# Optimization experiments

Hardware: AMD Instinct MI355X
Metric: run time of the kernel (lower is better)

Reference implementation:

```python
import jax, jax.numpy as jnp
import numpy as np

TEMPERATURE = 8.0  # sqrt(d_k=64)

def setup_inputs() -> dict:
    key = jax.random.key(0)
    kq, kk, kv = jax.random.split(key, 3)
    B, S, D = 32, 2048, 64  # B = batch*heads
    q = jax.random.normal(kq, (B, S, D), dtype=jnp.float32)
    k = jax.random.normal(kk, (B, S, D), dtype=jnp.float32)
    v = jax.random.normal(kv, (B, S, D), dtype=jnp.float32)
    return {"q": q, "k": k, "v": v}

def reference(q, k, v):
    # attn = softmax((q @ k^T) / temperature) along key dim; dropout = identity (eval)
    attn = jnp.einsum('bqd,bkd->bqk', q, k) / TEMPERATURE  # [B, S, S]
    attn = jax.nn.softmax(attn, axis=2)
    out = jnp.einsum('bqk,bkd->bqd', attn, v)              # [B, S, D]
    return out
```

## Files before the change

kernel.cpp:

```cpp
#include <hip/hip_runtime.h>
#include <stdint.h>


#define BATCH 32
#define SEQ   2048
#define DIM   64
#define QBLK_WAVE 32
#define NWAVES 4
#define QBLK  (QBLK_WAVE*NWAVES)
#define KVBLK 64
#define NT    (SEQ/KVBLK)
#define BUFSHORTS (KVBLK*DIM)

typedef __attribute__((ext_vector_type(8)))  __bf16   bf16x8;
typedef __attribute__((ext_vector_type(2)))  __bf16   bf16x2;
typedef __attribute__((ext_vector_type(16))) float    f32x16;
typedef __attribute__((ext_vector_type(2)))  unsigned uint2v;
typedef __attribute__((ext_vector_type(4)))  unsigned uint4v;

static __device__ __forceinline__ unsigned pk(float lo, float hi) {
    bf16x2 p; p[0] = (__bf16)lo; p[1] = (__bf16)hi;
    return __builtin_bit_cast(unsigned, p);
}
static __device__ __forceinline__ float exp2v(float x) {
    float r; asm("v_exp_f32 %0, %1" : "=v"(r) : "v"(x)); return r;
}
static __device__ __forceinline__ float max3(float a, float b, float c) {
    float d; asm("v_max3_f32 %0, %1, %2, %3" : "=v"(d) : "v"(a), "v"(b), "v"(c));
    return d;
}
static __device__ __forceinline__ float other_half(float v, int hi) {
    unsigned u = __builtin_bit_cast(unsigned, v);
    uint2v r = __builtin_amdgcn_permlane32_swap(u, u, false, false);
    return __builtin_bit_cast(float, hi ? r[0] : r[1]);
}

#define MFMA32(A, B, C) __builtin_amdgcn_mfma_f32_32x32x16_bf16((A), (B), (C), 0, 0, 0)
#define TRR(dst, OFFSTR) \
    asm volatile("ds_read_b64_tr_b16 %0, %1 offset:" OFFSTR : "=v"(dst) : "v"(trb))
#define SUM4(a,b,c,d) (((a)+(b)) + ((c)+(d)))

static __device__ __forceinline__ bf16x8 frag_of(uint2v r0, uint2v r1) {
    uint4v w = { r0[0], r0[1], r1[0], r1[1] };
    return __builtin_bit_cast(bf16x8, w);
}

__global__ __launch_bounds__(256, 2)
void attn_fwd_kernel(const float* __restrict__ q,
                     const float* __restrict__ k,
                     const float* __restrict__ v,
                     float* __restrict__ out)
{
    __shared__ unsigned short Ksh[2][BUFSHORTS];
    __shared__ unsigned short Vsh[2][BUFSHORTS];

    const int id    = blockIdx.x;
    const int swz   = (id & 7) * ((SEQ / QBLK) * BATCH / 8) + (id >> 3);
    const int batch = swz >> 4;
    const int qtile = swz & 15;

    const int t    = threadIdx.x;
    const int lane = t & 63;
    const int wid  = t >> 6;
    const int hi   = lane >> 5;
    const int l31  = lane & 31;
    const int l7   = lane & 7;

    const size_t bbase = (size_t)batch * SEQ * DIM;
    const int q0w = qtile * QBLK + wid * QBLK_WAVE;

    bf16x8 qf[4];
    {
        const float sc = 0.125f * 1.44269504088896341f;
        const float* qp = q + bbase + (size_t)(q0w + l31) * DIM + hi * 8;
        #pragma unroll
        for (int dblk = 0; dblk < 4; ++dblk) {
            float4 f0 = *(const float4*)(qp + dblk * 16);
            float4 f1 = *(const float4*)(qp + dblk * 16 + 4);
            uint4v w = { pk(f0.x * sc, f0.y * sc), pk(f0.z * sc, f0.w * sc),
                         pk(f1.x * sc, f1.y * sc), pk(f1.z * sc, f1.w * sc) };
            qf[dblk] = __builtin_bit_cast(bf16x8, w);
        }
    }
    asm("" : "+v"(qf[0]), "+v"(qf[1]), "+v"(qf[2]), "+v"(qf[3]));

    const int srow = t >> 2, sq = t & 3;
    const float* kg = k + bbase + (size_t)srow * DIM + sq * 16;
    const float* vg = v + bbase + (size_t)srow * DIM + sq * 16;
    const int ch0 = ((2 * sq)     ^ (srow & 7)) * 8;
    const int ch1 = ((2 * sq + 1) ^ (srow & 7)) * 8;

    const int bq = (l31 & 15) >> 2, ee = (lane >> 4) & 1, cc = lane & 3;
    const unsigned vb = (unsigned)(uintptr_t)&Vsh[0][0];
    const unsigned trbase = vb + (unsigned)((8 * hi + bq) * 128 +
                                            (((2 * ee + (cc >> 1)) ^ bq) * 16) + (cc & 1) * 8);

    f32x16 oacc0, oacc1;
    #pragma unroll
    for (int r = 0; r < 16; ++r) { oacc0[r] = 0.f; oacc1[r] = 0.f; }
    float m_run = 0.0f, l_run = 0.0f;

    float4 rk[4], rv[4];
    #pragma unroll
    for (int i = 0; i < 4; ++i) {
        rk[i] = *(const float4*)(kg + i * 4);
        rv[i] = *(const float4*)(vg + i * 4);
    }
    {
        uint4v kw0 = { pk(rk[0].x, rk[0].y), pk(rk[0].z, rk[0].w),
                       pk(rk[1].x, rk[1].y), pk(rk[1].z, rk[1].w) };
        uint4v kw1 = { pk(rk[2].x, rk[2].y), pk(rk[2].z, rk[2].w),
                       pk(rk[3].x, rk[3].y), pk(rk[3].z, rk[3].w) };
        uint4v vw0 = { pk(rv[0].x, rv[0].y), pk(rv[0].z, rv[0].w),
                       pk(rv[1].x, rv[1].y), pk(rv[1].z, rv[1].w) };
        uint4v vw1 = { pk(rv[2].x, rv[2].y), pk(rv[2].z, rv[2].w),
                       pk(rv[3].x, rv[3].y), pk(rv[3].z, rv[3].w) };
        *(uint4v*)&Ksh[0][srow * DIM + ch0] = kw0;
        *(uint4v*)&Ksh[0][srow * DIM + ch1] = kw1;
        *(uint4v*)&Vsh[0][srow * DIM + ch0] = vw0;
        *(uint4v*)&Vsh[0][srow * DIM + ch1] = vw1;
    }
    #pragma unroll
    for (int i = 0; i < 4; ++i) {
        rk[i] = *(const float4*)(kg + KVBLK * DIM + i * 4);
        rv[i] = *(const float4*)(vg + KVBLK * DIM + i * 4);
    }
    asm volatile("s_waitcnt lgkmcnt(0)" ::: "memory");

    #pragma unroll 2
    for (int tile = 0; tile < NT; ++tile) {
        const int cur = tile & 1;
        __builtin_amdgcn_s_barrier();
        __builtin_amdgcn_sched_barrier(0);

        const unsigned short* krow = &Ksh[cur][l31 * DIM];
        const unsigned trb = trbase + (unsigned)(cur * (2 * BUFSHORTS));

        f32x16 s0, s1;
        #pragma unroll
        for (int r = 0; r < 16; ++r) { s0[r] = 0.f; s1[r] = 0.f; }
        __builtin_amdgcn_s_setprio(1);
        #pragma unroll
        for (int dblk = 0; dblk < 4; ++dblk) {
            int cofs = (((2 * dblk + hi) ^ l7) * 8);
            bf16x8 kf0 = *(const bf16x8*)&krow[cofs];
            bf16x8 kf1 = *(const bf16x8*)&krow[32 * DIM + cofs];
            s0 = MFMA32(kf0, qf[dblk], s0);
            s1 = MFMA32(kf1, qf[dblk], s1);
        }
        __builtin_amdgcn_s_setprio(0);
        asm("" : "+v"(s0), "+v"(s1));

        if (tile + 1 < NT) {
            unsigned short* kst = &Ksh[cur ^ 1][srow * DIM];
            unsigned short* vst = &Vsh[cur ^ 1][srow * DIM];
            uint4v kw0 = { pk(rk[0].x, rk[0].y), pk(rk[0].z, rk[0].w),
                           pk(rk[1].x, rk[1].y), pk(rk[1].z, rk[1].w) };
            uint4v kw1 = { pk(rk[2].x, rk[2].y), pk(rk[2].z, rk[2].w),
                           pk(rk[3].x, rk[3].y), pk(rk[3].z, rk[3].w) };
            uint4v vw0 = { pk(rv[0].x, rv[0].y), pk(rv[0].z, rv[0].w),
                           pk(rv[1].x, rv[1].y), pk(rv[1].z, rv[1].w) };
            uint4v vw1 = { pk(rv[2].x, rv[2].y), pk(rv[2].z, rv[2].w),
                           pk(rv[3].x, rv[3].y), pk(rv[3].z, rv[3].w) };
            *(uint4v*)&kst[ch0] = kw0;
            *(uint4v*)&kst[ch1] = kw1;
            *(uint4v*)&vst[ch0] = vw0;
            *(uint4v*)&vst[ch1] = vw1;
        }

        uint2v m0k0r0, m0k0r1, m0k1r0, m0k1r1, m0k2r0, m0k2r1, m0k3r0, m0k3r1;
        uint2v m1k0r0, m1k0r1, m1k1r0, m1k1r1, m1k2r0, m1k2r1, m1k3r0, m1k3r1;
        TRR(m0k0r0, "0");    TRR(m0k0r1, "576");
        TRR(m0k1r0, "2048"); TRR(m0k1r1, "2624");
        TRR(m0k2r0, "4096"); TRR(m0k2r1, "4672");
        TRR(m0k3r0, "6144"); TRR(m0k3r1, "6720");
        TRR(m1k0r0, "64");   TRR(m1k0r1, "512");
        TRR(m1k1r0, "2112"); TRR(m1k1r1, "2560");
        TRR(m1k2r0, "4160"); TRR(m1k2r1, "4608");
        TRR(m1k3r0, "6208"); TRR(m1k3r1, "6656");

        {
            float t0 = max3(s0[0],  s0[1],  s0[2]);
            float t1 = max3(s0[3],  s0[4],  s0[5]);
            float t2 = max3(s0[6],  s0[7],  s0[8]);
            float t3 = max3(s0[9],  s0[10], s0[11]);
            float t4 = max3(s0[12], s0[13], s0[14]);
            float t5 = max3(s0[15], s1[0],  s1[1]);
            float t6 = max3(s1[2],  s1[3],  s1[4]);
            float t7 = max3(s1[5],  s1[6],  s1[7]);
            float t8 = max3(s1[8],  s1[9],  s1[10]);
            float t9 = max3(s1[11], s1[12], s1[13]);
            float ta = fmaxf(s1[14], s1[15]);
            float u0 = max3(t0, t1, t2);
            float u1 = max3(t3, t4, t5);
            float u2 = max3(t6, t7, t8);
            float u3 = max3(t9, ta, u0);
            float pmax = max3(u1, u2, u3);
            pmax = fmaxf(pmax, other_half(pmax, hi));
            if (!__all(pmax - m_run <= 12.0f)) {
                float mn    = fmaxf(m_run, pmax);
                float alpha = exp2v(m_run - mn);
                m_run = mn;
                l_run *= alpha;
                #pragma unroll
                for (int r = 0; r < 16; ++r) { oacc0[r] *= alpha; oacc1[r] *= alpha; }
            }
        }
        if (__all(m_run == 0.0f)) {
            #pragma unroll
            for (int r = 0; r < 16; ++r) s0[r] = exp2v(s0[r]);
            #pragma unroll
            for (int r = 0; r < 16; ++r) s1[r] = exp2v(s1[r]);
        } else {
            #pragma unroll
            for (int r = 0; r < 16; ++r) s0[r] = exp2v(s0[r] - m_run);
            #pragma unroll
            for (int r = 0; r < 16; ++r) s1[r] = exp2v(s1[r] - m_run);
        }
        {
            float a0 = SUM4(s0[0], s0[1], s0[2],  s0[3]);
            float a1 = SUM4(s0[4], s0[5], s0[6],  s0[7]);
            float a2 = SUM4(s0[8], s0[9], s0[10], s0[11]);
            float a3 = SUM4(s0[12], s0[13], s0[14], s0[15]);
            float b0 = SUM4(s1[0], s1[1], s1[2],  s1[3]);
            float b1 = SUM4(s1[4], s1[5], s1[6],  s1[7]);
            float b2 = SUM4(s1[8], s1[9], s1[10], s1[11]);
            float b3 = SUM4(s1[12], s1[13], s1[14], s1[15]);
            float rs = SUM4(SUM4(a0, a1, a2, a3), b0, b1, b2) + b3;
            rs += other_half(rs, hi);
            l_run += rs;
        }

        bf16x8 bfr0, bfr1, bfr2, bfr3;
        {
            uint2v x1 = __builtin_amdgcn_permlane32_swap(pk(s0[0], s0[1]),  pk(s0[4], s0[5]),  false, false);
            uint2v x2 = __builtin_amdgcn_permlane32_swap(pk(s0[2], s0[3]),  pk(s0[6], s0[7]),  false, false);
            uint4v w1 = { x1[0], x2[0], x1[1], x2[1] };
            bfr0 = __builtin_bit_cast(bf16x8, w1);
            uint2v y1 = __builtin_amdgcn_permlane32_swap(pk(s0[8], s0[9]),  pk(s0[12], s0[13]), false, false);
            uint2v y2 = __builtin_amdgcn_permlane32_swap(pk(s0[10], s0[11]), pk(s0[14], s0[15]), false, false);
            uint4v w2 = { y1[0], y2[0], y1[1], y2[1] };
            bfr1 = __builtin_bit_cast(bf16x8, w2);
            uint2v z1 = __builtin_amdgcn_permlane32_swap(pk(s1[0], s1[1]),  pk(s1[4], s1[5]),  false, false);
            uint2v z2 = __builtin_amdgcn_permlane32_swap(pk(s1[2], s1[3]),  pk(s1[6], s1[7]),  false, false);
            uint4v w3 = { z1[0], z2[0], z1[1], z2[1] };
            bfr2 = __builtin_bit_cast(bf16x8, w3);
            uint2v u1 = __builtin_amdgcn_permlane32_swap(pk(s1[8], s1[9]),  pk(s1[12], s1[13]), false, false);
            uint2v u2 = __builtin_amdgcn_permlane32_swap(pk(s1[10], s1[11]), pk(s1[14], s1[15]), false, false);
            uint4v w4 = { u1[0], u2[0], u1[1], u2[1] };
            bfr3 = __builtin_bit_cast(bf16x8, w4);
        }

        asm volatile("s_waitcnt lgkmcnt(0)" ::: "memory");
        __builtin_amdgcn_sched_barrier(0);

        __builtin_amdgcn_s_setprio(1);
        oacc0 = MFMA32(frag_of(m0k0r0, m0k0r1), bfr0, oacc0);
        oacc1 = MFMA32(frag_of(m1k0r0, m1k0r1), bfr0, oacc1);
        oacc0 = MFMA32(frag_of(m0k1r0, m0k1r1), bfr1, oacc0);
        oacc1 = MFMA32(frag_of(m1k1r0, m1k1r1), bfr1, oacc1);
        oacc0 = MFMA32(frag_of(m0k2r0, m0k2r1), bfr2, oacc0);
        oacc1 = MFMA32(frag_of(m1k2r0, m1k2r1), bfr2, oacc1);
        oacc0 = MFMA32(frag_of(m0k3r0, m0k3r1), bfr3, oacc0);
        oacc1 = MFMA32(frag_of(m1k3r0, m1k3r1), bfr3, oacc1);
        __builtin_amdgcn_s_setprio(0);

        if (tile + 2 < NT) {
            const float* kp = kg + (size_t)(tile + 2) * KVBLK * DIM;
            const float* vp = vg + (size_t)(tile + 2) * KVBLK * DIM;
            #pragma unroll
            for (int i = 0; i < 4; ++i) {
                rk[i] = *(const float4*)(kp + i * 4);
                rv[i] = *(const float4*)(vp + i * 4);
            }
        }
    }

    float invl = 1.0f / l_run;
    float* op = out + bbase + (size_t)(q0w + l31) * DIM + 4 * hi;
    #pragma unroll
    for (int rq = 0; rq < 4; ++rq) {
        float4 o0 = { oacc0[4 * rq] * invl, oacc0[4 * rq + 1] * invl,
                      oacc0[4 * rq + 2] * invl, oacc0[4 * rq + 3] * invl };
        float4 o1 = { oacc1[4 * rq] * invl, oacc1[4 * rq + 1] * invl,
                      oacc1[4 * rq + 2] * invl, oacc1[4 * rq + 3] * invl };
        *(float4*)(op + 8 * rq)      = o0;
        *(float4*)(op + 32 + 8 * rq) = o1;
    }
}

extern "C" void kernel_launch(void* const* d_in, const int* in_sizes, int n_in,
                              void* d_out, int out_size, void* d_ws, size_t ws_size,
                              hipStream_t stream) {
    const float* q = (const float*)d_in[0];
    const float* k = (const float*)d_in[1];
    const float* v = (const float*)d_in[2];
    float* out = (float*)d_out;
    dim3 grid((SEQ / QBLK) * BATCH);
    dim3 block(256);
    hipLaunchKernelGGL(attn_fwd_kernel, grid, block, 0, stream, q, k, v, out);
}
```

Baseline: 131.2 us.

## Split KV sequence across two blocks and merge partial softmax results

Adds a split-KV (flash-decoding style) path in which each query tile is processed by two blocks, each covering half of the key/value sequence. Partial unnormalized outputs and the row max and sum are written to workspace, and a separate combine kernel merges them. The K/V register prefetch is also restructured from two tiles ahead to one tile ahead, issued at the top of each iteration. The transpose LDS reads are split into two groups with partial lgkmcnt waits so the PV MFMAs can start earlier. This doubles the grid from 512 blocks to fill the GPU better, at the cost of a second launch and extra global traffic for the partial outputs.

Result: slower. 229.0 us (+74.6%).

```diff
diff --git a/kernel.cpp b/kernel.cpp
--- a/kernel.cpp
+++ b/kernel.cpp
@@ -9,8 +9,11 @@
 #define NWAVES 4
 #define QBLK  (QBLK_WAVE*NWAVES)
 #define KVBLK 64
-#define NT    (SEQ/KVBLK)
 #define BUFSHORTS (KVBLK*DIM)
+
+#define OFLOATS  (BATCH*SEQ*DIM)
+#define TOTQ     (BATCH*SEQ)
+#define WS_FLOATS (OFLOATS + 2*TOTQ + 2*TOTQ)
 
 typedef __attribute__((ext_vector_type(8)))  __bf16   bf16x8;
 typedef __attribute__((ext_vector_type(2)))  __bf16   bf16x2;
@@ -38,6 +41,9 @@
 #define MFMA32(A, B, C) __builtin_amdgcn_mfma_f32_32x32x16_bf16((A), (B), (C), 0, 0, 0)
 #define TRR(dst, OFFSTR) \
     asm volatile("ds_read_b64_tr_b16 %0, %1 offset:" OFFSTR : "=v"(dst) : "v"(trb))
+#define WAITL(NSTR) \
+    do { asm volatile("s_waitcnt lgkmcnt(" NSTR ")" ::: "memory"); \
+         __builtin_amdgcn_sched_barrier(0); } while (0)
 #define SUM4(a,b,c,d) (((a)+(b)) + ((c)+(d)))
 
 static __device__ __forceinline__ bf16x8 frag_of(uint2v r0, uint2v r1) {
@@ -45,19 +51,34 @@
     return __builtin_bit_cast(bf16x8, w);
 }
 
-__global__ __launch_bounds__(256, 2)
+template<bool SPLIT>
+__global__ __launch_bounds__(256, SPLIT ? 4 : 2)
 void attn_fwd_kernel(const float* __restrict__ q,
                      const float* __restrict__ k,
                      const float* __restrict__ v,
-                     float* __restrict__ out)
+                     float* __restrict__ out,
+                     float* __restrict__ wsO,
+                     float* __restrict__ wsL,
+                     float* __restrict__ wsM)
 {
+    constexpr int NT = SPLIT ? (SEQ / 2 / KVBLK) : (SEQ / KVBLK);
+
     __shared__ unsigned short Ksh[2][BUFSHORTS];
     __shared__ unsigned short Vsh[2][BUFSHORTS];
 
-    const int id    = blockIdx.x;
-    const int swz   = (id & 7) * ((SEQ / QBLK) * BATCH / 8) + (id >> 3);
-    const int batch = swz >> 4;
-    const int qtile = swz & 15;
+    const int id = blockIdx.x;
+    int batch, qtile, half;
+    if (SPLIT) {
+        const int swz = (id & 7) * 128 + (id >> 3);
+        batch = swz >> 5;
+        half  = (swz >> 4) & 1;
+        qtile = swz & 15;
+    } else {
+        const int swz = (id & 7) * 64 + (id >> 3);
+        batch = swz >> 4;
+        half  = 0;
+        qtile = swz & 15;
+    }
 
     const int t    = threadIdx.x;
     const int lane = t & 63;
@@ -67,6 +88,7 @@
     const int l7   = lane & 7;
 
     const size_t bbase = (size_t)batch * SEQ * DIM;
+    const size_t kvoff = bbase + (size_t)half * (SEQ / 2) * DIM;
     const int q0w = qtile * QBLK + wid * QBLK_WAVE;
 
     bf16x8 qf[4];
@@ -82,11 +104,10 @@
             qf[dblk] = __builtin_bit_cast(bf16x8, w);
         }
     }
-    asm("" : "+v"(qf[0]), "+v"(qf[1]), "+v"(qf[2]), "+v"(qf[3]));
 
     const int srow = t >> 2, sq = t & 3;
-    const float* kg = k + bbase + (size_t)srow * DIM + sq * 16;
-    const float* vg = v + bbase + (size_t)srow * DIM + sq * 16;
+    const float* kg = k + kvoff + (size_t)srow * DIM + sq * 16;
+    const float* vg = v + kvoff + (size_t)srow * DIM + sq * 16;
     const int ch0 = ((2 * sq)     ^ (srow & 7)) * 8;
     const int ch1 = ((2 * sq + 1) ^ (srow & 7)) * 8;
 
@@ -100,30 +121,19 @@
     for (int r = 0; r < 16; ++r) { oacc0[r] = 0.f; oacc1[r] = 0.f; }
     float m_run = 0.0f, l_run = 0.0f;
 
-    float4 rk[4], rv[4];
-    #pragma unroll
-    for (int i = 0; i < 4; ++i) {
-        rk[i] = *(const float4*)(kg + i * 4);
-        rv[i] = *(const float4*)(vg + i * 4);
-    }
     {
-        uint4v kw0 = { pk(rk[0].x, rk[0].y), pk(rk[0].z, rk[0].w),
-                       pk(rk[1].x, rk[1].y), pk(rk[1].z, rk[1].w) };
-        uint4v kw1 = { pk(rk[2].x, rk[2].y), pk(rk[2].z, rk[2].w),
-                       pk(rk[3].x, rk[3].y), pk(rk[3].z, rk[3].w) };
-        uint4v vw0 = { pk(rv[0].x, rv[0].y), pk(rv[0].z, rv[0].w),
-                       pk(rv[1].x, rv[1].y), pk(rv[1].z, rv[1].w) };
-        uint4v vw1 = { pk(rv[2].x, rv[2].y), pk(rv[2].z, rv[2].w),
-                       pk(rv[3].x, rv[3].y), pk(rv[3].z, rv[3].w) };
+        float4 a0 = *(const float4*)(kg + 0),  a1 = *(const float4*)(kg + 4);
+        float4 a2 = *(const float4*)(kg + 8),  a3 = *(const float4*)(kg + 12);
+        float4 b0 = *(const float4*)(vg + 0),  b1 = *(const float4*)(vg + 4);
+        float4 b2 = *(const float4*)(vg + 8),  b3 = *(const float4*)(vg + 12);
+        uint4v kw0 = { pk(a0.x, a0.y), pk(a0.z, a0.w), pk(a1.x, a1.y), pk(a1.z, a1.w) };
+        uint4v kw1 = { pk(a2.x, a2.y), pk(a2.z, a2.w), pk(a3.x, a3.y), pk(a3.z, a3.w) };
+        uint4v vw0 = { pk(b0.x, b0.y), pk(b0.z, b0.w), pk(b1.x, b1.y), pk(b1.z, b1.w) };
+        uint4v vw1 = { pk(b2.x, b2.y), pk(b2.z, b2.w), pk(b3.x, b3.y), pk(b3.z, b3.w) };
         *(uint4v*)&Ksh[0][srow * DIM + ch0] = kw0;
         *(uint4v*)&Ksh[0][srow * DIM + ch1] = kw1;
         *(uint4v*)&Vsh[0][srow * DIM + ch0] = vw0;
         *(uint4v*)&Vsh[0][srow * DIM + ch1] = vw1;
-    }
-    #pragma unroll
-    for (int i = 0; i < 4; ++i) {
-        rk[i] = *(const float4*)(kg + KVBLK * DIM + i * 4);
-        rv[i] = *(const float4*)(vg + KVBLK * DIM + i * 4);
     }
     asm volatile("s_waitcnt lgkmcnt(0)" ::: "memory");
 
@@ -135,6 +145,17 @@
 
         const unsigned short* krow = &Ksh[cur][l31 * DIM];
         const unsigned trb = trbase + (unsigned)(cur * (2 * BUFSHORTS));
+        const bool haveNext = (tile + 1 < NT);
+
+        float4 a0, a1, a2, a3, b0, b1, b2, b3;
+        if (haveNext) {
+            const float* kp = kg + (size_t)(tile + 1) * KVBLK * DIM;
+            const float* vp = vg + (size_t)(tile + 1) * KVBLK * DIM;
+            a0 = *(const float4*)(kp + 0);  a1 = *(const float4*)(kp + 4);
+            a2 = *(const float4*)(kp + 8);  a3 = *(const float4*)(kp + 12);
+            b0 = *(const float4*)(vp + 0);  b1 = *(const float4*)(vp + 4);
+            b2 = *(const float4*)(vp + 8);  b3 = *(const float4*)(vp + 12);
+        }
 
         f32x16 s0, s1;
         #pragma unroll
@@ -149,35 +170,25 @@
             s1 = MFMA32(kf1, qf[dblk], s1);
         }
         __builtin_amdgcn_s_setprio(0);
-        asm("" : "+v"(s0), "+v"(s1));
-
-        if (tile + 1 < NT) {
+
+        if (haveNext) {
             unsigned short* kst = &Ksh[cur ^ 1][srow * DIM];
             unsigned short* vst = &Vsh[cur ^ 1][srow * DIM];
-            uint4v kw0 = { pk(rk[0].x, rk[0].y), pk(rk[0].z, rk[0].w),
-                           pk(rk[1].x, rk[1].y), pk(rk[1].z, rk[1].w) };
-            uint4v kw1 = { pk(rk[2].x, rk[2].y), pk(rk[2].z, rk[2].w),
-                           pk(rk[3].x, rk[3].y), pk(rk[3].z, rk[3].w) };
-            uint4v vw0 = { pk(rv[0].x, rv[0].y), pk(rv[0].z, rv[0].w),
-                           pk(rv[1].x, rv[1].y), pk(rv[1].z, rv[1].w) };
-            uint4v vw1 = { pk(rv[2].x, rv[2].y), pk(rv[2].z, rv[2].w),
-                           pk(rv[3].x, rv[3].y), pk(rv[3].z, rv[3].w) };
+            uint4v kw0 = { pk(a0.x, a0.y), pk(a0.z, a0.w), pk(a1.x, a1.y), pk(a1.z, a1.w) };
+            uint4v kw1 = { pk(a2.x, a2.y), pk(a2.z, a2.w), pk(a3.x, a3.y), pk(a3.z, a3.w) };
+            uint4v vw0 = { pk(b0.x, b0.y), pk(b0.z, b0.w), pk(b1.x, b1.y), pk(b1.z, b1.w) };
+            uint4v vw1 = { pk(b2.x, b2.y), pk(b2.z, b2.w), pk(b3.x, b3.y), pk(b3.z, b3.w) };
             *(uint4v*)&kst[ch0] = kw0;
             *(uint4v*)&kst[ch1] = kw1;
             *(uint4v*)&vst[ch0] = vw0;
             *(uint4v*)&vst[ch1] = vw1;
         }
 
-        uint2v m0k0r0, m0k0r1, m0k1r0, m0k1r1, m0k2r0, m0k2r1, m0k3r0, m0k3r1;
-        uint2v m1k0r0, m1k0r1, m1k1r0, m1k1r1, m1k2r0, m1k2r1, m1k3r0, m1k3r1;
-        TRR(m0k0r0, "0");    TRR(m0k0r1, "576");
-        TRR(m0k1r0, "2048"); TRR(m0k1r1, "2624");
-        TRR(m0k2r0, "4096"); TRR(m0k2r1, "4672");
-        TRR(m0k3r0, "6144"); TRR(m0k3r1, "6720");
-        TRR(m1k0r0, "64");   TRR(m1k0r1, "512");
-        TRR(m1k1r0, "2112"); TRR(m1k1r1, "2560");
-        TRR(m1k2r0, "4160"); TRR(m1k2r1, "4608");
-        TRR(m1k3r0, "6208"); TRR(m1k3r1, "6656");
+        uint2v a00, a01, a10, a11, c00, c01, c10, c11;
+        TRR(a00, "0");    TRR(a01, "576");
+        TRR(c00, "64");   TRR(c01, "512");
+        TRR(a10, "2048"); TRR(a11, "2624");
+        TRR(c10, "2112"); TRR(c11, "2560");
 
         {
             float t0 = max3(s0[0],  s0[1],  s0[2]);
@@ -218,15 +229,15 @@
             for (int r = 0; r < 16; ++r) s1[r] = exp2v(s1[r] - m_run);
         }
         {
-            float a0 = SUM4(s0[0], s0[1], s0[2],  s0[3]);
-            float a1 = SUM4(s0[4], s0[5], s0[6],  s0[7]);
-            float a2 = SUM4(s0[8], s0[9], s0[10], s0[11]);
-            float a3 = SUM4(s0[12], s0[13], s0[14], s0[15]);
-            float b0 = SUM4(s1[0], s1[1], s1[2],  s1[3]);
-            float b1 = SUM4(s1[4], s1[5], s1[6],  s1[7]);
-            float b2 = SUM4(s1[8], s1[9], s1[10], s1[11]);
-            float b3 = SUM4(s1[12], s1[13], s1[14], s1[15]);
-            float rs = SUM4(SUM4(a0, a1, a2, a3), b0, b1, b2) + b3;
+            float x0 = SUM4(s0[0], s0[1], s0[2],  s0[3]);
+            float x1 = SUM4(s0[4], s0[5], s0[6],  s0[7]);
+            float x2 = SUM4(s0[8], s0[9], s0[10], s0[11]);
+            float x3 = SUM4(s0[12], s0[13], s0[14], s0[15]);
+            float y0 = SUM4(s1[0], s1[1], s1[2],  s1[3]);
+            float y1 = SUM4(s1[4], s1[5], s1[6],  s1[7]);
+            float y2 = SUM4(s1[8], s1[9], s1[10], s1[11]);
+            float y3 = SUM4(s1[12], s1[13], s1[14], s1[15]);
+            float rs = SUM4(SUM4(x0, x1, x2, x3), y0, y1, y2) + y3;
             rs += other_half(rs, hi);
             l_run += rs;
         }
@@ -251,41 +262,79 @@
             bfr3 = __builtin_bit_cast(bf16x8, w4);
         }
 
-        asm volatile("s_waitcnt lgkmcnt(0)" ::: "memory");
-        __builtin_amdgcn_sched_barrier(0);
+        uint2v a20, a21, a30, a31, c20, c21, c30, c31;
+        TRR(a20, "4096"); TRR(a21, "4672");
+        TRR(c20, "4160"); TRR(c21, "4608");
+        TRR(a30, "6144"); TRR(a31, "6720");
+        TRR(c30, "6208"); TRR(c31, "6656");
 
         __builtin_amdgcn_s_setprio(1);
-        oacc0 = MFMA32(frag_of(m0k0r0, m0k0r1), bfr0, oacc0);
-        oacc1 = MFMA32(frag_of(m1k0r0, m1k0r1), bfr0, oacc1);
-        oacc0 = MFMA32(frag_of(m0k1r0, m0k1r1), bfr1, oacc0);
-        oacc1 = MFMA32(frag_of(m1k1r0, m1k1r1), bfr1, oacc1);
-        oacc0 = MFMA32(frag_of(m0k2r0, m0k2r1), bfr2, oacc0);
-        oacc1 = MFMA32(frag_of(m1k2r0, m1k2r1), bfr2, oacc1);
-        oacc0 = MFMA32(frag_of(m0k3r0, m0k3r1), bfr3, oacc0);
-        oacc1 = MFMA32(frag_of(m1k3r0, m1k3r1), bfr3, oacc1);
+        WAITL("8");
+        oacc0 = MFMA32(frag_of(a00, a01), bfr0, oacc0);
+        oacc1 = MFMA32(frag_of(c00, c01), bfr0, oacc1);
+        oacc0 = MFMA32(frag_of(a10, a11), bfr1, oacc0);
+        oacc1 = MFMA32(frag_of(c10, c11), bfr1, oacc1);
+        WAITL("0");
+        oacc0 = MFMA32(frag_of(a20, a21), bfr2, oacc0);
+        oacc1 = MFMA32(frag_of(c20, c21), bfr2, oacc1);
+        oacc0 = MFMA32(frag_of(a30, a31), bfr3, oacc0);
+        oacc1 = MFMA32(frag_of(c30, c31), bfr3, oacc1);
         __builtin_amdgcn_s_setprio(0);
-
-        if (tile + 2 < NT) {
-            const float* kp = kg + (size_t)(tile + 2) * KVBLK * DIM;
-            const float* vp = vg + (size_t)(tile + 2) * KVBLK * DIM;
-            #pragma unroll
-            for (int i = 0; i < 4; ++i) {
-                rk[i] = *(const float4*)(kp + i * 4);
-                rv[i] = *(const float4*)(vp + i * 4);
-            }
-        }
-    }
-
-    float invl = 1.0f / l_run;
-    float* op = out + bbase + (size_t)(q0w + l31) * DIM + 4 * hi;
-    #pragma unroll
-    for (int rq = 0; rq < 4; ++rq) {
-        float4 o0 = { oacc0[4 * rq] * invl, oacc0[4 * rq + 1] * invl,
-                      oacc0[4 * rq + 2] * invl, oacc0[4 * rq + 3] * invl };
-        float4 o1 = { oacc1[4 * rq] * invl, oacc1[4 * rq + 1] * invl,
-                      oacc1[4 * rq + 2] * invl, oacc1[4 * rq + 3] * invl };
-        *(float4*)(op + 8 * rq)      = o0;
-        *(float4*)(op + 32 + 8 * rq) = o1;
+    }
+
+    const int qrow = q0w + l31;
+    if (SPLIT) {
+        float* opart = half ? wsO : out;
+        float* op = opart + bbase + (size_t)qrow * DIM + 4 * hi;
+        #pragma unroll
+        for (int rq = 0; rq < 4; ++rq) {
+            float4 o0 = { oacc0[4 * rq], oacc0[4 * rq + 1],
+                          oacc0[4 * rq + 2], oacc0[4 * rq + 3] };
+            float4 o1 = { oacc1[4 * rq], oacc1[4 * rq + 1],
+                          oacc1[4 * rq + 2], oacc1[4 * rq + 3] };
+            *(float4*)(op + 8 * rq)      = o0;
+            *(float4*)(op + 32 + 8 * rq) = o1;
+        }
+        if (hi == 0) {
+            const int lin = half * TOTQ + batch * SEQ + qrow;
+            wsL[lin] = l_run;
+            wsM[lin] = m_run;
+        }
+    } else {
+        float invl = 1.0f / l_run;
+        float* op = out + bbase + (size_t)qrow * DIM + 4 * hi;
+        #pragma unroll
+        for (int rq = 0; rq < 4; ++rq) {
+            float4 o0 = { oacc0[4 * rq] * invl, oacc0[4 * rq + 1] * invl,
+                          oacc0[4 * rq + 2] * invl, oacc0[4 * rq + 3] * invl };
+            float4 o1 = { oacc1[4 * rq] * invl, oacc1[4 * rq + 1] * invl,
+                          oacc1[4 * rq + 2] * invl, oacc1[4 * rq + 3] * invl };
+            *(float4*)(op + 8 * rq)      = o0;
+            *(float4*)(op + 32 + 8 * rq) = o1;
+        }
+    }
+}
+
+__global__ __launch_bounds__(256)
+void combine_kernel(float* __restrict__ out, const float* __restrict__ O2,
+                    const float* __restrict__ wsL, const float* __restrict__ wsM)
+{
+    constexpr int TOT4 = OFLOATS / 4;
+    for (int i = blockIdx.x * blockDim.x + threadIdx.x; i < TOT4;
+         i += gridDim.x * blockDim.x) {
+        const int qg = i >> 4;
+        float l1 = wsL[qg], l2 = wsL[TOTQ + qg];
+        float m1 = wsM[qg], m2 = wsM[TOTQ + qg];
+        float M  = fmaxf(m1, m2);
+        float e1 = exp2f(m1 - M), e2 = exp2f(m2 - M);
+        float inv = 1.0f / (e1 * l1 + e2 * l2);
+        float4 o1 = ((const float4*)out)[i];
+        float4 o2 = ((const float4*)O2)[i];
+        float4 r = { (e1 * o1.x + e2 * o2.x) * inv,
+                     (e1 * o1.y + e2 * o2.y) * inv,
+                     (e1 * o1.z + e2 * o2.z) * inv,
+                     (e1 * o1.w + e2 * o2.w) * inv };
+        ((float4*)out)[i] = r;
     }
 }
 
@@ -296,7 +345,19 @@
     const float* k = (const float*)d_in[1];
     const float* v = (const float*)d_in[2];
     float* out = (float*)d_out;
-    dim3 grid((SEQ / QBLK) * BATCH);
-    dim3 block(256);
-    hipLaunchKernelGGL(attn_fwd_kernel, grid, block, 0, stream, q, k, v, out);
-}
+    float* wsO = (float*)d_ws;
+    float* wsL = wsO + OFLOATS;
+    float* wsM = wsL + 2 * TOTQ;
+    const bool split = ws_size >= (size_t)WS_FLOATS * sizeof(float);
+    if (split) {
+        dim3 grid(2 * (SEQ / QBLK) * BATCH);
+        hipLaunchKernelGGL((attn_fwd_kernel<true>), grid, dim3(256), 0, stream,
+                           q, k, v, out, wsO, wsL, wsM);
+        hipLaunchKernelGGL(combine_kernel, dim3(2048), dim3(256), 0, stream,
+                           out, wsO, wsL, wsM);
+    } else {
+        dim3 grid((SEQ / QBLK) * BATCH);
+        hipLaunchKernelGGL((attn_fwd_kernel<false>), grid, dim3(256), 0, stream,
+                           q, k, v, out, wsO, wsL, wsM);
+    }
+}
```
